# Kernel optimization log

Measured on AMD Instinct MI355X. Metric: run time of the kernel, lower is better.

Reference implementation:

```python
import jax, jax.numpy as jnp
import numpy as np

B, C, L, K, R = 32, 64, 16384, 3, 8

def _lrelu(x):
    return jnp.where(x >= 0, x, 0.1 * x)

def setup_inputs() -> dict:
    key = jax.random.key(0)
    ks = jax.random.split(key, 8)
    s = lambda i, shape: (jax.random.normal(ks[i], shape, jnp.float32) * 0.05)
    return {
        "x0": jax.random.normal(ks[0], (B, C, L), jnp.float32),
        "x1": jax.random.normal(ks[1], (B, 64), jnp.float32),
        "W1": s(2, (64, 64)),           # Linear(64,64).weight [out,in]
        "W2": s(3, (64 * K, 64)),       # Linear(64,64*K).weight
        "conv_w": s(4, (C, C)),         # 1x1 Conv1d weight [out,in]
        "conv_b": s(5, (C,)),
        "ca_w1": s(6, (C // R, C)),     # CA conv1 weight
        "ca_w2": s(7, (C, C // R)),     # CA conv2 weight
    }

def reference(x0, x1, W1, W2, conv_w, conv_b, ca_w1, ca_w2):
    b, c, l = x0.shape
    k = W2.shape[0] // 64
    pad = (k - 1) // 2
    # dynamic per-(b,c) depthwise kernels
    h = _lrelu(x1 @ W1.T)                         # [b,64]
    kern = (h @ W2.T).reshape(b, c, k)            # [b,c,k]
    # depthwise conv1d (cross-correlation), groups=b*c
    xp = jnp.pad(x0, ((0, 0), (0, 0), (pad, pad)))
    out = sum(xp[:, :, j:j + l] * kern[:, :, j:j + 1] for j in range(k))
    out = _lrelu(out)
    # 1x1 conv
    out = jnp.einsum('bcl,oc->bol', out, conv_w) + conv_b[None, :, None]
    # channel attention gate on x1
    att = jax.nn.sigmoid(_lrelu(x1 @ ca_w1.T) @ ca_w2.T)  # [b,c]
    return out + x0 * att[:, :, None]
```

## Files before the change

kernel.cpp:

```cpp
#include <hip/hip_runtime.h>
#include <math.h>

#define B_ 32
#define C_ 64
#define L_ 16384
#define LT 64
#define NBLK (B_ * (L_ / LT))

typedef __attribute__((ext_vector_type(8))) short short8;
typedef __attribute__((ext_vector_type(4))) float f32x4;

__device__ __forceinline__ unsigned short f2bf(float x) {
  unsigned int u = __builtin_bit_cast(unsigned int, x);
  u += 0x7fffu + ((u >> 16) & 1u);
  return (unsigned short)(u >> 16);
}

__device__ __forceinline__ float lrelu(float x) {
  return x >= 0.f ? x : 0.1f * x;
}

__device__ __forceinline__ void load_lds_16(const void* g, void* l) {
  __builtin_amdgcn_global_load_lds(
      (const __attribute__((address_space(1))) void*)g,
      (__attribute__((address_space(3))) void*)l, 16, 0, 0);
}

__global__ void da_prep(const float* __restrict__ x1,
                        const float* __restrict__ W1,
                        const float* __restrict__ W2,
                        const float* __restrict__ ca_w1,
                        const float* __restrict__ ca_w2,
                        const float* __restrict__ conv_w,
                        float* __restrict__ kern4,
                        float* __restrict__ att,
                        unsigned short* __restrict__ wfrag) {
  int b = blockIdx.x;
  int t = threadIdx.x;
  __shared__ float x1s[64], h[64], a1[8];
  x1s[t] = x1[b * 64 + t];
  __syncthreads();
  {
    const float* w1r = W1 + t * 64;
    float s = 0.f;
    #pragma unroll
    for (int i = 0; i < 64; ++i) s = fmaf(x1s[i], w1r[i], s);
    h[t] = lrelu(s);
  }
  if (t < 8) {
    const float* cw = ca_w1 + t * 64;
    float a = 0.f;
    #pragma unroll
    for (int i = 0; i < 64; ++i) a = fmaf(x1s[i], cw[i], a);
    a1[t] = lrelu(a);
  }
  __syncthreads();
  #pragma unroll
  for (int kk = 0; kk < 3; ++kk) {
    const float* w2r = W2 + (t * 3 + kk) * 64;
    float s2 = 0.f;
    #pragma unroll
    for (int i = 0; i < 64; ++i) s2 = fmaf(h[i], w2r[i], s2);
    kern4[(b * 64 + t) * 4 + kk] = s2;
  }
  kern4[(b * 64 + t) * 4 + 3] = 0.f;
  {
    float a = 0.f;
    #pragma unroll
    for (int r = 0; r < 8; ++r) a = fmaf(a1[r], ca_w2[t * 8 + r], a);
    att[b * 64 + t] = 1.f / (1.f + expf(-a));
  }
  if (b == 0) {
    #pragma unroll
    for (int kt = 0; kt < 2; ++kt)
      #pragma unroll
      for (int mt = 0; mt < 4; ++mt)
        #pragma unroll
        for (int j = 0; j < 8; ++j) {
          float e = conv_w[(mt * 16 + (t & 15)) * 64 + kt * 32 + (t >> 4) * 8 + j];
          wfrag[(((kt * 4 + mt) * 64) + t) * 8 + j] = f2bf(e);
        }
  }
}

__global__ __launch_bounds__(256, 6) void da_main(
    const float* __restrict__ x0,
    const float* __restrict__ conv_b,
    const float* __restrict__ kern4,
    const float* __restrict__ att,
    const unsigned short* __restrict__ wfrag,
    float* __restrict__ out) {
  __shared__ float x0s[64 * LT];
  __shared__ unsigned short midT[LT * 64];
  __shared__ float cbs[64], atts[64];

  int bid = blockIdx.x;
  int b = bid >> 8;
  int l0 = (bid & 255) * LT;
  int tid = threadIdx.x;
  int lane = tid & 63;
  int wave = tid >> 6;

  int m_lane = lane & 15;
  int kbase = (lane >> 4) * 8;

  const float* xb = x0 + (size_t)(b * 64) * L_;

  {
    int p = lane & 15;
    int r4 = lane >> 4;
    #pragma unroll
    for (int i = 0; i < 4; ++i) {
      int c = wave * 16 + i * 4 + r4;
      const float* g = xb + (size_t)c * L_ + l0 + ((p ^ (c & 7)) << 2);
      load_lds_16(g, &x0s[(wave * 16 + i * 4) * LT]);
    }
  }

  short8 af[2][4];
  #pragma unroll
  for (int kt = 0; kt < 2; ++kt)
    #pragma unroll
    for (int mt = 0; mt < 4; ++mt)
      af[kt][mt] = *(const short8*)&wfrag[(((kt * 4 + mt) * 64) + lane) * 8];

  float4 kv = *(const float4*)&kern4[(b * 64 + lane) * 4];
  float k0 = kv.x, k1 = kv.y, k2 = kv.z;

  float hp = 0.f, hn = 0.f;
  if (wave == 0 && l0 > 0) hp = xb[(size_t)lane * L_ + l0 - 1];
  if (wave == 3 && l0 + LT < L_) hn = xb[(size_t)lane * L_ + l0 + LT];

  if (tid < 64) {
    cbs[tid] = conv_b[tid];
    atts[tid] = att[b * 64 + tid];
  }

  __syncthreads();

  {
    int c = lane;
    int w0 = wave * 16;
    const float* row = &x0s[c * LT];
    const int csw = (c & 7) << 2;

    float4 q[4];
    #pragma unroll
    for (int i = 0; i < 4; ++i)
      q[i] = *(const float4*)&row[((wave * 4 + i) ^ (c & 7)) << 2];

    float prev, nxt;
    if (wave == 0) {
      prev = hp;
    } else {
      int w = w0 - 1;
      prev = row[((w & ~3) ^ csw) + (w & 3)];
    }
    if (wave == 3) {
      nxt = hn;
    } else {
      int w = w0 + 16;
      nxt = row[((w & ~3) ^ csw) + (w & 3)];
    }

    #pragma unroll
    for (int i = 0; i < 4; ++i) {
      float xa = q[i].x, xb2 = q[i].y, xc = q[i].z, xd = q[i].w;
      float xm1 = prev;
      if (i > 0) xm1 = q[i - 1].w;
      float xp1 = nxt;
      if (i < 3) xp1 = q[i + 1].x;
      float m0 = fmaf(k0, xm1, fmaf(k1, xa,  k2 * xb2));
      float m1 = fmaf(k0, xa,  fmaf(k1, xb2, k2 * xc));
      float m2 = fmaf(k0, xb2, fmaf(k1, xc,  k2 * xd));
      float m3 = fmaf(k0, xc,  fmaf(k1, xd,  k2 * xp1));
      int l = w0 + 4 * i;
      midT[(l + 0) * 64 + (c ^ (((l + 0) & 7) << 3))] = f2bf(lrelu(m0));
      midT[(l + 1) * 64 + (c ^ (((l + 1) & 7) << 3))] = f2bf(lrelu(m1));
      midT[(l + 2) * 64 + (c ^ (((l + 2) & 7) << 3))] = f2bf(lrelu(m2));
      midT[(l + 3) * 64 + (c ^ (((l + 3) & 7) << 3))] = f2bf(lrelu(m3));
    }
  }
  __syncthreads();

  f32x4 acc[4];
  #pragma unroll
  for (int mt = 0; mt < 4; ++mt) acc[mt] = (f32x4){0.f, 0.f, 0.f, 0.f};
  int lw = wave * 16;
  #pragma unroll
  for (int kt = 0; kt < 2; ++kt) {
    int l = lw + m_lane;
    int cb = kt * 32 + kbase;
    const short8 bf = *(const short8*)&midT[l * 64 + (cb ^ ((l & 7) << 3))];
    #pragma unroll
    for (int mt = 0; mt < 4; ++mt)
      acc[mt] = __builtin_amdgcn_mfma_f32_16x16x32_bf16(af[kt][mt], bf,
                                                        acc[mt], 0, 0, 0);
  }

  {
    int r0 = (lane >> 4) * 4;
    int w = lw + m_lane;
    #pragma unroll
    for (int mt = 0; mt < 4; ++mt) {
      #pragma unroll
      for (int r = 0; r < 4; ++r) {
        int o = mt * 16 + r0 + r;
        float xv = x0s[o * LT + (((w & ~3) ^ ((o & 7) << 2)) + (w & 3))];
        out[(size_t)(b * 64 + o) * L_ + l0 + w] =
            acc[mt][r] + cbs[o] + xv * atts[o];
      }
    }
  }
}

extern "C" void kernel_launch(void* const* d_in, const int* in_sizes, int n_in,
                              void* d_out, int out_size, void* d_ws, size_t ws_size,
                              hipStream_t stream) {
  const float* x0     = (const float*)d_in[0];
  const float* x1     = (const float*)d_in[1];
  const float* W1     = (const float*)d_in[2];
  const float* W2     = (const float*)d_in[3];
  const float* conv_w = (const float*)d_in[4];
  const float* conv_b = (const float*)d_in[5];
  const float* ca_w1  = (const float*)d_in[6];
  const float* ca_w2  = (const float*)d_in[7];
  float* out = (float*)d_out;

  float* kern4 = (float*)d_ws;
  float* att   = kern4 + B_ * C_ * 4;
  unsigned short* wfrag = (unsigned short*)(att + B_ * C_);

  da_prep<<<dim3(B_), dim3(64), 0, stream>>>(x1, W1, W2, ca_w1, ca_w2, conv_w,
                                             kern4, att, wfrag);
  da_main<<<dim3(NBLK), dim3(256), 0, stream>>>(x0, conv_b, kern4, att, wfrag,
                                                out);
}
```

Measured before the change: 73.88 us.

## Drop LDS staging of x0 and block barriers in main kernel

Each lane now loads its channel's 16-element x0 segment, plus halo values, straight from global memory into registers, instead of staging the tile in LDS with global_load_lds. The depthwise conv results go into midT and are read back only by the same wave, so both __syncthreads are removed. The residual x0, conv_b and att values are re-read from global in the epilogue, and the occupancy hint rises from 6 to 7. This cuts LDS use and barriers, but x0 loads become strided across lanes and x0 is read twice from global/cache.

```diff
diff --git a/kernel.cpp b/kernel.cpp
--- a/kernel.cpp
+++ b/kernel.cpp
@@ -18,12 +18,6 @@
 
 __device__ __forceinline__ float lrelu(float x) {
   return x >= 0.f ? x : 0.1f * x;
-}
-
-__device__ __forceinline__ void load_lds_16(const void* g, void* l) {
-  __builtin_amdgcn_global_load_lds(
-      (const __attribute__((address_space(1))) void*)g,
-      (__attribute__((address_space(3))) void*)l, 16, 0, 0);
 }
 
 __global__ void da_prep(const float* __restrict__ x1,
@@ -83,16 +77,14 @@
   }
 }
 
-__global__ __launch_bounds__(256, 6) void da_main(
+__global__ __launch_bounds__(256, 7) void da_main(
     const float* __restrict__ x0,
     const float* __restrict__ conv_b,
     const float* __restrict__ kern4,
     const float* __restrict__ att,
     const unsigned short* __restrict__ wfrag,
     float* __restrict__ out) {
-  __shared__ float x0s[64 * LT];
   __shared__ unsigned short midT[LT * 64];
-  __shared__ float cbs[64], atts[64];
 
   int bid = blockIdx.x;
   int b = bid >> 8;
@@ -103,17 +95,40 @@
 
   int m_lane = lane & 15;
   int kbase = (lane >> 4) * 8;
+  int qq = lane >> 4;
 
-  const float* xb = x0 + (size_t)(b * 64) * L_;
+  int c = lane;
+  int gl = l0 + wave * 16;
+
+  const float* xrow = x0 + ((size_t)(b * 64 + c)) * L_ + gl;
+  float4 q0 = ((const float4*)xrow)[0];
+  float4 q1 = ((const float4*)xrow)[1];
+  float4 q2 = ((const float4*)xrow)[2];
+  float4 q3 = ((const float4*)xrow)[3];
+  float hp = (gl > 0) ? xrow[-1] : 0.f;
+  float hn = (gl + 16 < L_) ? xrow[16] : 0.f;
+
+  float4 kv = *(const float4*)&kern4[(b * 64 + c) * 4];
+  float k0 = kv.x, k1 = kv.y, k2 = kv.z;
 
   {
-    int p = lane & 15;
-    int r4 = lane >> 4;
+    float4 q[4] = {q0, q1, q2, q3};
     #pragma unroll
     for (int i = 0; i < 4; ++i) {
-      int c = wave * 16 + i * 4 + r4;
-      const float* g = xb + (size_t)c * L_ + l0 + ((p ^ (c & 7)) << 2);
-      load_lds_16(g, &x0s[(wave * 16 + i * 4) * LT]);
+      float xa = q[i].x, xb2 = q[i].y, xc = q[i].z, xd = q[i].w;
+      float xm1 = hp;
+      if (i > 0) xm1 = q[i - 1].w;
+      float xp1 = hn;
+      if (i < 3) xp1 = q[i + 1].x;
+      float m0 = fmaf(k0, xm1, fmaf(k1, xa,  k2 * xb2));
+      float m1 = fmaf(k0, xa,  fmaf(k1, xb2, k2 * xc));
+      float m2 = fmaf(k0, xb2, fmaf(k1, xc,  k2 * xd));
+      float m3 = fmaf(k0, xc,  fmaf(k1, xd,  k2 * xp1));
+      int l = wave * 16 + 4 * i;
+      midT[(l + 0) * 64 + (c ^ (((l + 0) & 7) << 3))] = f2bf(lrelu(m0));
+      midT[(l + 1) * 64 + (c ^ (((l + 1) & 7) << 3))] = f2bf(lrelu(m1));
+      midT[(l + 2) * 64 + (c ^ (((l + 2) & 7) << 3))] = f2bf(lrelu(m2));
+      midT[(l + 3) * 64 + (c ^ (((l + 3) & 7) << 3))] = f2bf(lrelu(m3));
     }
   }
 
@@ -124,72 +139,12 @@
     for (int mt = 0; mt < 4; ++mt)
       af[kt][mt] = *(const short8*)&wfrag[(((kt * 4 + mt) * 64) + lane) * 8];
 
-  float4 kv = *(const float4*)&kern4[(b * 64 + lane) * 4];
-  float k0 = kv.x, k1 = kv.y, k2 = kv.z;
-
-  float hp = 0.f, hn = 0.f;
-  if (wave == 0 && l0 > 0) hp = xb[(size_t)lane * L_ + l0 - 1];
-  if (wave == 3 && l0 + LT < L_) hn = xb[(size_t)lane * L_ + l0 + LT];
-
-  if (tid < 64) {
-    cbs[tid] = conv_b[tid];
-    atts[tid] = att[b * 64 + tid];
-  }
-
-  __syncthreads();
-
-  {
-    int c = lane;
-    int w0 = wave * 16;
-    const float* row = &x0s[c * LT];
-    const int csw = (c & 7) << 2;
-
-    float4 q[4];
-    #pragma unroll
-    for (int i = 0; i < 4; ++i)
-      q[i] = *(const float4*)&row[((wave * 4 + i) ^ (c & 7)) << 2];
-
-    float prev, nxt;
-    if (wave == 0) {
-      prev = hp;
-    } else {
-      int w = w0 - 1;
-      prev = row[((w & ~3) ^ csw) + (w & 3)];
-    }
-    if (wave == 3) {
-      nxt = hn;
-    } else {
-      int w = w0 + 16;
-      nxt = row[((w & ~3) ^ csw) + (w & 3)];
-    }
-
-    #pragma unroll
-    for (int i = 0; i < 4; ++i) {
-      float xa = q[i].x, xb2 = q[i].y, xc = q[i].z, xd = q[i].w;
-      float xm1 = prev;
-      if (i > 0) xm1 = q[i - 1].w;
-      float xp1 = nxt;
-      if (i < 3) xp1 = q[i + 1].x;
-      float m0 = fmaf(k0, xm1, fmaf(k1, xa,  k2 * xb2));
-      float m1 = fmaf(k0, xa,  fmaf(k1, xb2, k2 * xc));
-      float m2 = fmaf(k0, xb2, fmaf(k1, xc,  k2 * xd));
-      float m3 = fmaf(k0, xc,  fmaf(k1, xd,  k2 * xp1));
-      int l = w0 + 4 * i;
-      midT[(l + 0) * 64 + (c ^ (((l + 0) & 7) << 3))] = f2bf(lrelu(m0));
-      midT[(l + 1) * 64 + (c ^ (((l + 1) & 7) << 3))] = f2bf(lrelu(m1));
-      midT[(l + 2) * 64 + (c ^ (((l + 2) & 7) << 3))] = f2bf(lrelu(m2));
-      midT[(l + 3) * 64 + (c ^ (((l + 3) & 7) << 3))] = f2bf(lrelu(m3));
-    }
-  }
-  __syncthreads();
-
   f32x4 acc[4];
   #pragma unroll
   for (int mt = 0; mt < 4; ++mt) acc[mt] = (f32x4){0.f, 0.f, 0.f, 0.f};
-  int lw = wave * 16;
+  int l = wave * 16 + m_lane;
   #pragma unroll
   for (int kt = 0; kt < 2; ++kt) {
-    int l = lw + m_lane;
     int cb = kt * 32 + kbase;
     const short8 bf = *(const short8*)&midT[l * 64 + (cb ^ ((l & 7) << 3))];
     #pragma unroll
@@ -199,16 +154,15 @@
   }
 
   {
-    int r0 = (lane >> 4) * 4;
-    int w = lw + m_lane;
+    int w = wave * 16 + m_lane;
     #pragma unroll
     for (int mt = 0; mt < 4; ++mt) {
       #pragma unroll
       for (int r = 0; r < 4; ++r) {
-        int o = mt * 16 + r0 + r;
-        float xv = x0s[o * LT + (((w & ~3) ^ ((o & 7) << 2)) + (w & 3))];
-        out[(size_t)(b * 64 + o) * L_ + l0 + w] =
-            acc[mt][r] + cbs[o] + xv * atts[o];
+        int o = mt * 16 + qq * 4 + r;
+        float xv = x0[((size_t)(b * 64 + o)) * L_ + l0 + w];
+        out[((size_t)(b * 64 + o)) * L_ + l0 + w] =
+            acc[mt][r] + conv_b[o] + xv * att[b * 64 + o];
       }
     }
   }
```

New measurement: 95.94 us. 1.3x slower.

## Process four L-tiles per block with double-buffered async LDS prefetch

Applied to the files above, without the earlier changes.

Each block now loops over four consecutive 64-wide L tiles. It prefetches the next tile of x0 (plus its right halo) into a second LDS buffer via global_load_lds while the current tile is convolved, multiplied on MFMA and stored. Manual vmcnt waits and barriers replace the per-block __syncthreads, and the left halo is passed between tiles through LDS. Block IDs are also remapped across groups of eight, and bias and attention values are kept in registers. This is meant to overlap load latency with compute and stores, at the cost of lower occupancy (launch bounds 3), fewer blocks, and fragile hand-counted waitcnt values.

```diff
diff --git a/kernel.cpp b/kernel.cpp
--- a/kernel.cpp
+++ b/kernel.cpp
@@ -5,7 +5,8 @@
 #define C_ 64
 #define L_ 16384
 #define LT 64
-#define NBLK (B_ * (L_ / LT))
+#define NT 4
+#define NBLK (B_ * (L_ / (LT * NT)))
 
 typedef __attribute__((ext_vector_type(8))) short short8;
 typedef __attribute__((ext_vector_type(4))) float f32x4;
@@ -24,6 +25,11 @@
   __builtin_amdgcn_global_load_lds(
       (const __attribute__((address_space(1))) void*)g,
       (__attribute__((address_space(3))) void*)l, 16, 0, 0);
+}
+__device__ __forceinline__ void load_lds_4(const void* g, void* l) {
+  __builtin_amdgcn_global_load_lds(
+      (const __attribute__((address_space(1))) void*)g,
+      (__attribute__((address_space(3))) void*)l, 4, 0, 0);
 }
 
 __global__ void da_prep(const float* __restrict__ x1,
@@ -83,39 +89,47 @@
   }
 }
 
-__global__ __launch_bounds__(256, 6) void da_main(
+__global__ __launch_bounds__(256, 3) void da_main(
     const float* __restrict__ x0,
     const float* __restrict__ conv_b,
     const float* __restrict__ kern4,
     const float* __restrict__ att,
     const unsigned short* __restrict__ wfrag,
     float* __restrict__ out) {
-  __shared__ float x0s[64 * LT];
+  __shared__ float x0s[2][64 * LT];
   __shared__ unsigned short midT[LT * 64];
-  __shared__ float cbs[64], atts[64];
-
-  int bid = blockIdx.x;
-  int b = bid >> 8;
-  int l0 = (bid & 255) * LT;
+  __shared__ float haloL[2][64], haloR[2][64];
+
+  int hw = blockIdx.x;
+  int bid = (hw & 7) * (NBLK / 8) + (hw >> 3);
+  int b = bid >> 6;
+  int base_l = (bid & 63) * (NT * LT);
   int tid = threadIdx.x;
   int lane = tid & 63;
   int wave = tid >> 6;
 
   int m_lane = lane & 15;
   int kbase = (lane >> 4) * 8;
+  int qq = lane >> 4;
 
   const float* xb = x0 + (size_t)(b * 64) * L_;
 
-  {
+  auto STAGE = [&](int t1, int d) {
     int p = lane & 15;
-    int r4 = lane >> 4;
+    int r4r = lane >> 4;
     #pragma unroll
     for (int i = 0; i < 4; ++i) {
-      int c = wave * 16 + i * 4 + r4;
-      const float* g = xb + (size_t)c * L_ + l0 + ((p ^ (c & 7)) << 2);
-      load_lds_16(g, &x0s[(wave * 16 + i * 4) * LT]);
-    }
-  }
+      int c = wave * 16 + i * 4 + r4r;
+      const float* g = xb + (size_t)c * L_ + base_l + t1 * LT + ((p ^ (c & 7)) << 2);
+      load_lds_16(g, &x0s[d][(wave * 16 + i * 4) * LT]);
+    }
+  };
+  auto HALO = [&](int t1) {
+    int l = base_l + (t1 + 1) * LT;
+    if (l >= L_) l = base_l;
+    const float* g = xb + (size_t)lane * L_ + l;
+    load_lds_4(g, &haloR[t1 & 1][0]);
+  };
 
   short8 af[2][4];
   #pragma unroll
@@ -127,89 +141,125 @@
   float4 kv = *(const float4*)&kern4[(b * 64 + lane) * 4];
   float k0 = kv.x, k1 = kv.y, k2 = kv.z;
 
-  float hp = 0.f, hn = 0.f;
-  if (wave == 0 && l0 > 0) hp = xb[(size_t)lane * L_ + l0 - 1];
-  if (wave == 3 && l0 + LT < L_) hn = xb[(size_t)lane * L_ + l0 + LT];
-
-  if (tid < 64) {
-    cbs[tid] = conv_b[tid];
-    atts[tid] = att[b * 64 + tid];
-  }
-
-  __syncthreads();
-
-  {
-    int c = lane;
-    int w0 = wave * 16;
-    const float* row = &x0s[c * LT];
-    const int csw = (c & 7) << 2;
-
-    float4 q[4];
-    #pragma unroll
-    for (int i = 0; i < 4; ++i)
-      q[i] = *(const float4*)&row[((wave * 4 + i) ^ (c & 7)) << 2];
-
-    float prev, nxt;
-    if (wave == 0) {
-      prev = hp;
+  float cb_r[4][4], at_r[4][4];
+  #pragma unroll
+  for (int mt = 0; mt < 4; ++mt)
+    #pragma unroll
+    for (int r = 0; r < 4; ++r) {
+      int o = mt * 16 + qq * 4 + r;
+      cb_r[mt][r] = conv_b[o];
+      at_r[mt][r] = att[b * 64 + o];
+    }
+
+  float hl0 = 0.f;
+  if (wave == 0 && base_l > 0) hl0 = xb[(size_t)lane * L_ + base_l - 1];
+
+  asm volatile("s_waitcnt vmcnt(0)" ::: "memory");
+  if (wave == 0) haloL[0][lane] = hl0;
+  asm volatile("s_waitcnt lgkmcnt(0)" ::: "memory");
+
+  STAGE(0, 0);
+  if (wave == 0) HALO(0);
+
+  #pragma unroll
+  for (int t = 0; t < NT; ++t) {
+    const int d = t & 1;
+
+    if (t + 1 < NT) {
+      STAGE(t + 1, d ^ 1);
+      if (wave == 0) HALO(t + 1);
+    }
+
+    if (t == 0) {
+      if (wave == 0) asm volatile("s_waitcnt vmcnt(5)" ::: "memory");
+      else           asm volatile("s_waitcnt vmcnt(4)" ::: "memory");
+    } else if (t < NT - 1) {
+      if (wave == 0) asm volatile("s_waitcnt vmcnt(21)" ::: "memory");
+      else           asm volatile("s_waitcnt vmcnt(20)" ::: "memory");
     } else {
-      int w = w0 - 1;
-      prev = row[((w & ~3) ^ csw) + (w & 3)];
-    }
-    if (wave == 3) {
-      nxt = hn;
-    } else {
-      int w = w0 + 16;
-      nxt = row[((w & ~3) ^ csw) + (w & 3)];
-    }
-
-    #pragma unroll
-    for (int i = 0; i < 4; ++i) {
-      float xa = q[i].x, xb2 = q[i].y, xc = q[i].z, xd = q[i].w;
-      float xm1 = prev;
-      if (i > 0) xm1 = q[i - 1].w;
-      float xp1 = nxt;
-      if (i < 3) xp1 = q[i + 1].x;
-      float m0 = fmaf(k0, xm1, fmaf(k1, xa,  k2 * xb2));
-      float m1 = fmaf(k0, xa,  fmaf(k1, xb2, k2 * xc));
-      float m2 = fmaf(k0, xb2, fmaf(k1, xc,  k2 * xd));
-      float m3 = fmaf(k0, xc,  fmaf(k1, xd,  k2 * xp1));
-      int l = w0 + 4 * i;
-      midT[(l + 0) * 64 + (c ^ (((l + 0) & 7) << 3))] = f2bf(lrelu(m0));
-      midT[(l + 1) * 64 + (c ^ (((l + 1) & 7) << 3))] = f2bf(lrelu(m1));
-      midT[(l + 2) * 64 + (c ^ (((l + 2) & 7) << 3))] = f2bf(lrelu(m2));
-      midT[(l + 3) * 64 + (c ^ (((l + 3) & 7) << 3))] = f2bf(lrelu(m3));
-    }
-  }
-  __syncthreads();
-
-  f32x4 acc[4];
-  #pragma unroll
-  for (int mt = 0; mt < 4; ++mt) acc[mt] = (f32x4){0.f, 0.f, 0.f, 0.f};
-  int lw = wave * 16;
-  #pragma unroll
-  for (int kt = 0; kt < 2; ++kt) {
-    int l = lw + m_lane;
-    int cb = kt * 32 + kbase;
-    const short8 bf = *(const short8*)&midT[l * 64 + (cb ^ ((l & 7) << 3))];
-    #pragma unroll
-    for (int mt = 0; mt < 4; ++mt)
-      acc[mt] = __builtin_amdgcn_mfma_f32_16x16x32_bf16(af[kt][mt], bf,
-                                                        acc[mt], 0, 0, 0);
-  }
-
-  {
-    int r0 = (lane >> 4) * 4;
-    int w = lw + m_lane;
-    #pragma unroll
-    for (int mt = 0; mt < 4; ++mt) {
-      #pragma unroll
-      for (int r = 0; r < 4; ++r) {
-        int o = mt * 16 + r0 + r;
-        float xv = x0s[o * LT + (((w & ~3) ^ ((o & 7) << 2)) + (w & 3))];
-        out[(size_t)(b * 64 + o) * L_ + l0 + w] =
-            acc[mt][r] + cbs[o] + xv * atts[o];
-      }
+      asm volatile("s_waitcnt vmcnt(16)" ::: "memory");
+    }
+    __builtin_amdgcn_s_barrier();
+
+    {
+      int c = lane;
+      int w0 = wave * 16;
+      const float* row = &x0s[d][c * LT];
+      const int csw = (c & 7) << 2;
+
+      float4 q[4];
+      #pragma unroll
+      for (int i = 0; i < 4; ++i)
+        q[i] = *(const float4*)&row[((wave * 4 + i) ^ (c & 7)) << 2];
+
+      float prev, nxt;
+      if (wave == 0) {
+        prev = haloL[d][c];
+      } else {
+        int w = w0 - 1;
+        prev = row[((w & ~3) ^ csw) + (w & 3)];
+      }
+      if (wave == 3) {
+        bool oobR = (base_l + (t + 1) * LT) >= L_;
+        nxt = oobR ? 0.f : haloR[d][c];
+      } else {
+        int w = w0 + 16;
+        nxt = row[((w & ~3) ^ csw) + (w & 3)];
+      }
+
+      if (t + 1 < NT && wave == 3) haloL[d ^ 1][c] = q[3].w;
+
+      #pragma unroll
+      for (int i = 0; i < 4; ++i) {
+        float xa = q[i].x, xb2 = q[i].y, xc = q[i].z, xd = q[i].w;
+        float xm1 = prev;
+        if (i > 0) xm1 = q[i - 1].w;
+        float xp1 = nxt;
+        if (i < 3) xp1 = q[i + 1].x;
+        float m0 = fmaf(k0, xm1, fmaf(k1, xa,  k2 * xb2));
+        float m1 = fmaf(k0, xa,  fmaf(k1, xb2, k2 * xc));
+        float m2 = fmaf(k0, xb2, fmaf(k1, xc,  k2 * xd));
+        float m3 = fmaf(k0, xc,  fmaf(k1, xd,  k2 * xp1));
+        int l = w0 + 4 * i;
+        midT[(l + 0) * 64 + (c ^ (((l + 0) & 7) << 3))] = f2bf(lrelu(m0));
+        midT[(l + 1) * 64 + (c ^ (((l + 1) & 7) << 3))] = f2bf(lrelu(m1));
+        midT[(l + 2) * 64 + (c ^ (((l + 2) & 7) << 3))] = f2bf(lrelu(m2));
+        midT[(l + 3) * 64 + (c ^ (((l + 3) & 7) << 3))] = f2bf(lrelu(m3));
+      }
+    }
+
+    f32x4 acc[4];
+    #pragma unroll
+    for (int mt = 0; mt < 4; ++mt) acc[mt] = (f32x4){0.f, 0.f, 0.f, 0.f};
+    int l = wave * 16 + m_lane;
+    #pragma unroll
+    for (int kt = 0; kt < 2; ++kt) {
+      int cb = kt * 32 + kbase;
+      const short8 bf = *(const short8*)&midT[l * 64 + (cb ^ ((l & 7) << 3))];
+      #pragma unroll
+      for (int mt = 0; mt < 4; ++mt)
+        acc[mt] = __builtin_amdgcn_mfma_f32_16x16x32_bf16(af[kt][mt], bf,
+                                                          acc[mt], 0, 0, 0);
+    }
+
+    {
+      int w = wave * 16 + m_lane;
+      int l0t = base_l + t * LT;
+      #pragma unroll
+      for (int mt = 0; mt < 4; ++mt) {
+        #pragma unroll
+        for (int r = 0; r < 4; ++r) {
+          int o = mt * 16 + qq * 4 + r;
+          float xv = x0s[d][o * LT + (((w & ~3) ^ ((o & 7) << 2)) + (w & 3))];
+          out[(size_t)(b * 64 + o) * L_ + l0t + w] =
+              acc[mt][r] + cb_r[mt][r] + xv * at_r[mt][r];
+        }
+      }
+    }
+
+    if (t + 1 < NT) {
+      asm volatile("s_waitcnt lgkmcnt(0)" ::: "memory");
+      __builtin_amdgcn_s_barrier();
     }
   }
 }
```

Result: slower. 97.76 us (+32.3%).
